# Performance work log

Measured on AMD Instinct MI355X. Metric: run time of the kernel, lower is better.

Reference implementation:

```python
import jax, jax.numpy as jnp
import numpy as np

IN_FEATURES = 4096
OUT_FEATURES = 16384
SCALE = 0.02


def setup_inputs() -> dict:
    key = jax.random.key(0)
    kx, kw, kb = jax.random.split(key, 3)
    x = jax.random.normal(kx, (4, 2048, IN_FEATURES), dtype=jnp.float32)
    # int8-valued quantized weight, stored as int32 (values in [-127, 127])
    q_weight = jax.random.randint(kw, (OUT_FEATURES, IN_FEATURES), -127, 128, dtype=jnp.int32)
    scale = jnp.float32(SCALE)
    bias = jax.random.normal(kb, (OUT_FEATURES,), dtype=jnp.float32)
    return {"x": x, "q_weight": q_weight, "scale": scale, "bias": bias}


def reference(x, q_weight, scale, bias):
    # weight = q_weight.float() * scale  (dequantize)
    weight = q_weight.astype(jnp.float32) * scale  # [out, in]
    # F.linear(x, weight, bias) = x @ weight.T + bias
    out = jnp.einsum('bsi,oi->bso', x, weight) + bias
    return out
```

## Files before the change

kernel.cpp:

```cpp
#include <hip/hip_runtime.h>
#include <stdint.h>

#define K_DIM 4096
#define N_DIM 16384
#define M_DIM 8192

typedef _Float16 half8 __attribute__((ext_vector_type(8)));
typedef float floatx4 __attribute__((ext_vector_type(4)));

__device__ inline void gld_lds16(const void* g, void* l) {
  __builtin_amdgcn_global_load_lds(
      (const __attribute__((address_space(1))) void*)g,
      (__attribute__((address_space(3))) void*)l, 16, 0, 0);
}

__global__ __launch_bounds__(256) void cvt_f32_f16_k(const float* __restrict__ in,
                                                     _Float16* __restrict__ out) {
  size_t idx = (size_t)blockIdx.x * 256 + threadIdx.x;
  const float4* p = (const float4*)in + idx * 2;
  float4 v0 = p[0], v1 = p[1];
  half8 h;
  h[0] = (_Float16)v0.x; h[1] = (_Float16)v0.y; h[2] = (_Float16)v0.z; h[3] = (_Float16)v0.w;
  h[4] = (_Float16)v1.x; h[5] = (_Float16)v1.y; h[6] = (_Float16)v1.z; h[7] = (_Float16)v1.w;
  *((half8*)out + idx) = h;
}

__global__ __launch_bounds__(256) void cvt_i32_f16_k(const int* __restrict__ in,
                                                     _Float16* __restrict__ out) {
  size_t idx = (size_t)blockIdx.x * 256 + threadIdx.x;
  const int4* p = (const int4*)in + idx * 2;
  int4 v0 = p[0], v1 = p[1];
  half8 h;
  h[0] = (_Float16)v0.x; h[1] = (_Float16)v0.y; h[2] = (_Float16)v0.z; h[3] = (_Float16)v0.w;
  h[4] = (_Float16)v1.x; h[5] = (_Float16)v1.y; h[6] = (_Float16)v1.z; h[7] = (_Float16)v1.w;
  *((half8*)out + idx) = h;
}

template <bool FROM_WS>
__global__ __launch_bounds__(256) void qgemm_k(const void* __restrict__ Av,
                                               const void* __restrict__ Bv,
                                               const float* __restrict__ scale_p,
                                               const float* __restrict__ bias,
                                               float* __restrict__ out) {
  constexpr int BK = 64;
  __shared__ __align__(16) _Float16 sA[128 * BK];
  __shared__ __align__(16) _Float16 sB[128 * BK];

  const int tid  = threadIdx.x;
  const int lane = tid & 63;
  const int wid  = tid >> 6;
  const int wm   = wid >> 1, wn = wid & 1;
  const int q    = lane >> 4;
  const int l15  = lane & 15;
  const int bn   = blockIdx.x, bm = blockIdx.y;

  int gI[4], rI[4], cI[4];
#pragma unroll
  for (int p = 0; p < 4; ++p) {
    int g = p * 256 + tid;
    gI[p] = g;
    rI[p] = g >> 3;
    cI[p] = (g & 7) ^ (rI[p] & 7);
  }

  floatx4 acc[4][4] = {};

  const int arow = wm * 64 + l15;
  const int brow = wn * 64 + l15;

  const _Float16* Ah = nullptr; const _Float16* Bh = nullptr;
  const float* Af = nullptr;    const int* Bq = nullptr;
  if constexpr (FROM_WS) { Ah = (const _Float16*)Av; Bh = (const _Float16*)Bv; }
  else                   { Af = (const float*)Av;    Bq = (const int*)Bv; }

#pragma unroll 1
  for (int k0 = 0; k0 < K_DIM; k0 += BK) {
    if constexpr (FROM_WS) {
#pragma unroll
      for (int p = 0; p < 4; ++p)
        gld_lds16(Ah + (size_t)(bm * 128 + rI[p]) * K_DIM + k0 + cI[p] * 8,
                  &sA[gI[p] * 8]);
#pragma unroll
      for (int p = 0; p < 4; ++p)
        gld_lds16(Bh + (size_t)(bn * 128 + rI[p]) * K_DIM + k0 + cI[p] * 8,
                  &sB[gI[p] * 8]);
    } else {
#pragma unroll
      for (int p = 0; p < 4; ++p) {
        const float4* pa =
            (const float4*)(Af + (size_t)(bm * 128 + rI[p]) * K_DIM + k0 + cI[p] * 8);
        float4 v0 = pa[0], v1 = pa[1];
        half8 h;
        h[0] = (_Float16)v0.x; h[1] = (_Float16)v0.y; h[2] = (_Float16)v0.z; h[3] = (_Float16)v0.w;
        h[4] = (_Float16)v1.x; h[5] = (_Float16)v1.y; h[6] = (_Float16)v1.z; h[7] = (_Float16)v1.w;
        *(half8*)&sA[gI[p] * 8] = h;
      }
#pragma unroll
      for (int p = 0; p < 4; ++p) {
        const int4* pb =
            (const int4*)(Bq + (size_t)(bn * 128 + rI[p]) * K_DIM + k0 + cI[p] * 8);
        int4 v0 = pb[0], v1 = pb[1];
        half8 h;
        h[0] = (_Float16)v0.x; h[1] = (_Float16)v0.y; h[2] = (_Float16)v0.z; h[3] = (_Float16)v0.w;
        h[4] = (_Float16)v1.x; h[5] = (_Float16)v1.y; h[6] = (_Float16)v1.z; h[7] = (_Float16)v1.w;
        *(half8*)&sB[gI[p] * 8] = h;
      }
    }
    __syncthreads();

#pragma unroll
    for (int kk = 0; kk < BK; kk += 32) {
      const int xt = ((((kk >> 3) + q) ^ (lane & 7)) * 8);
      half8 af[4], bf[4];
#pragma unroll
      for (int i = 0; i < 4; ++i) af[i] = *(const half8*)&sA[(arow + i * 16) * BK + xt];
#pragma unroll
      for (int j = 0; j < 4; ++j) bf[j] = *(const half8*)&sB[(brow + j * 16) * BK + xt];
#pragma unroll
      for (int i = 0; i < 4; ++i)
#pragma unroll
        for (int j = 0; j < 4; ++j)
          acc[i][j] = __builtin_amdgcn_mfma_f32_16x16x32_f16(af[i], bf[j], acc[i][j], 0, 0, 0);
    }
    __syncthreads();
  }

  const float s = *scale_p;
  float bv[4];
#pragma unroll
  for (int j = 0; j < 4; ++j) bv[j] = bias[bn * 128 + wn * 64 + j * 16 + l15];
  const int mb = bm * 128 + wm * 64 + q * 4;
  const size_t nb = (size_t)bn * 128 + wn * 64 + l15;
#pragma unroll
  for (int i = 0; i < 4; ++i) {
#pragma unroll
    for (int j = 0; j < 4; ++j) {
      size_t off = (size_t)(mb + i * 16) * N_DIM + nb + j * 16;
      floatx4 c = acc[i][j];
      out[off]             = c[0] * s + bv[j];
      out[off + N_DIM]     = c[1] * s + bv[j];
      out[off + 2 * N_DIM] = c[2] * s + bv[j];
      out[off + 3 * N_DIM] = c[3] * s + bv[j];
    }
  }
}

extern "C" void kernel_launch(void* const* d_in, const int* in_sizes, int n_in,
                              void* d_out, int out_size, void* d_ws, size_t ws_size,
                              hipStream_t stream) {
  const float* x     = (const float*)d_in[0];
  const int*   qw    = (const int*)d_in[1];
  const float* scale = (const float*)d_in[2];
  const float* bias  = (const float*)d_in[3];
  float* out = (float*)d_out;

  const size_t xs  = (size_t)M_DIM * K_DIM;
  const size_t wsz = (size_t)N_DIM * K_DIM;
  const size_t need = (xs + wsz) * sizeof(_Float16);

  dim3 grid(N_DIM / 128, M_DIM / 128);
  if (ws_size >= need) {
    _Float16* xh = (_Float16*)d_ws;
    _Float16* wh = xh + xs;
    cvt_f32_f16_k<<<(int)(xs / 8 / 256), 256, 0, stream>>>(x, xh);
    cvt_i32_f16_k<<<(int)(wsz / 8 / 256), 256, 0, stream>>>(qw, wh);
    qgemm_k<true><<<grid, 256, 0, stream>>>(xh, wh, scale, bias, out);
  } else {
    qgemm_k<false><<<grid, 256, 0, stream>>>(x, qw, scale, bias, out);
  }
}
```

Measured before the change: 2.129 ms.

## Add 256x256 double-buffered GEMM kernel with interleaved async LDS staging

Adds a new fp16 MFMA GEMM kernel for the workspace path. It uses 256x256 tiles with 512 threads and double-buffered LDS. Global-to-LDS loads for the next tiles are interleaved between MFMA phases, with explicit waitcnt, barriers and setprio. It also remaps block indices to improve L2 reuse. The aim is to raise arithmetic intensity and hide memory latency behind compute, at the cost of 128KB of LDS, heavy register use, and many barriers per iteration.

```diff
diff --git a/kernel.cpp b/kernel.cpp
--- a/kernel.cpp
+++ b/kernel.cpp
@@ -36,6 +36,139 @@
   *((half8*)out + idx) = h;
 }
 
+__global__ __launch_bounds__(512, 2) void qgemm256_k(
+    const _Float16* __restrict__ Ah, const _Float16* __restrict__ Bh,
+    const float* __restrict__ scale_p, const float* __restrict__ bias,
+    float* __restrict__ out) {
+  constexpr int BK = 64;
+  constexpr int NT = K_DIM / BK;
+  __shared__ __align__(16) _Float16 sA[2][256 * BK];
+  __shared__ __align__(16) _Float16 sB[2][256 * BK];
+
+  const int tid  = threadIdx.x;
+  const int lane = tid & 63;
+  const int wid  = tid >> 6;
+  const int wm   = wid >> 2;
+  const int wn   = wid & 3;
+  const int q    = lane >> 4;
+  const int l15  = lane & 15;
+
+  const int nbn = N_DIM / 256;
+  int lin = blockIdx.y * gridDim.x + blockIdx.x;
+  int swz = (lin & 7) * ((M_DIM / 256) * nbn / 8) + (lin >> 3);
+  const int bn = swz % nbn;
+  const int bm = swz / nbn;
+
+  const int s_slot = tid & 7;
+  const int r0     = tid >> 3;
+  const int cc     = s_slot ^ (r0 & 7);
+  const _Float16* Agp = Ah + (size_t)(bm * 256 + r0) * K_DIM + cc * 8;
+  const _Float16* Bgp = Bh + (size_t)(bn * 256 + r0) * K_DIM + cc * 8;
+
+#define STAGE_A(b, tt, h)                                                        \
+  { const _Float16* s_ = Agp + (size_t)(h) * 128 * K_DIM + (tt) * BK;            \
+    gld_lds16(s_, &sA[(b)][(h) * 8192 + tid * 8]);                               \
+    gld_lds16(s_ + (size_t)64 * K_DIM, &sA[(b)][(h) * 8192 + 4096 + tid * 8]); }
+#define STAGE_B(b, tt, h)                                                        \
+  { const _Float16* s_ = Bgp + (size_t)(h) * 128 * K_DIM + (tt) * BK;            \
+    gld_lds16(s_, &sB[(b)][(h) * 8192 + tid * 8]);                               \
+    gld_lds16(s_ + (size_t)64 * K_DIM, &sB[(b)][(h) * 8192 + 4096 + tid * 8]); }
+#define MFMA16(d, a_, b_) d = __builtin_amdgcn_mfma_f32_16x16x32_f16(a_, b_, d, 0, 0, 0)
+#define SBAR() __builtin_amdgcn_sched_barrier(0)
+#define BARRIER() { SBAR(); __builtin_amdgcn_s_barrier(); SBAR(); }
+
+  const int rbA = (wm * 128 + l15) * BK;
+  const int rbB = (wn * 64 + l15) * BK;
+  const int xt0 = (q ^ (l15 & 7)) * 8;
+  const int xt1 = ((q + 4) ^ (l15 & 7)) * 8;
+
+  floatx4 acc[8][4] = {};
+
+  STAGE_A(0, 0, 0); STAGE_A(0, 0, 1);
+  STAGE_B(0, 0, 0); STAGE_B(0, 0, 1);
+  STAGE_A(1, 1, 0); STAGE_A(1, 1, 1);
+  asm volatile("s_waitcnt vmcnt(4)" ::: "memory");
+  BARRIER();
+
+#pragma unroll 1
+  for (int t = 0; t < NT; ++t) {
+    const int buf = t & 1;
+    const _Float16* pa = sA[buf];
+    const _Float16* pb = sB[buf];
+    half8 a0[8], a1[8], b0[4], b1[4];
+
+    b0[0] = *(const half8*)&pb[rbB + xt0];
+    b0[1] = *(const half8*)&pb[rbB + 1024 + xt0];
+#pragma unroll
+    for (int i = 0; i < 8; ++i) a0[i] = *(const half8*)&pa[rbA + i * 1024 + xt0];
+    if (t < NT - 1) STAGE_B(buf ^ 1, t + 1, 0);
+    BARRIER();
+    __builtin_amdgcn_s_setprio(1);
+#pragma unroll
+    for (int i = 0; i < 8; ++i) { MFMA16(acc[i][0], a0[i], b0[0]); MFMA16(acc[i][1], a0[i], b0[1]); }
+    __builtin_amdgcn_s_setprio(0);
+    BARRIER();
+
+    b0[2] = *(const half8*)&pb[rbB + 2048 + xt0];
+    b0[3] = *(const half8*)&pb[rbB + 3072 + xt0];
+#pragma unroll
+    for (int i = 0; i < 8; ++i) a1[i] = *(const half8*)&pa[rbA + i * 1024 + xt1];
+    if (t < NT - 1) STAGE_B(buf ^ 1, t + 1, 1);
+    BARRIER();
+    __builtin_amdgcn_s_setprio(1);
+#pragma unroll
+    for (int i = 0; i < 8; ++i) { MFMA16(acc[i][2], a0[i], b0[2]); MFMA16(acc[i][3], a0[i], b0[3]); }
+    __builtin_amdgcn_s_setprio(0);
+    BARRIER();
+
+    b1[0] = *(const half8*)&pb[rbB + xt1];
+    b1[1] = *(const half8*)&pb[rbB + 1024 + xt1];
+    if (t < NT - 2) STAGE_A(buf, t + 2, 0);
+    BARRIER();
+    __builtin_amdgcn_s_setprio(1);
+#pragma unroll
+    for (int i = 0; i < 8; ++i) { MFMA16(acc[i][0], a1[i], b1[0]); MFMA16(acc[i][1], a1[i], b1[1]); }
+    __builtin_amdgcn_s_setprio(0);
+    BARRIER();
+
+    b1[2] = *(const half8*)&pb[rbB + 2048 + xt1];
+    b1[3] = *(const half8*)&pb[rbB + 3072 + xt1];
+    if (t < NT - 2) STAGE_A(buf, t + 2, 1);
+    BARRIER();
+    __builtin_amdgcn_s_setprio(1);
+#pragma unroll
+    for (int i = 0; i < 8; ++i) { MFMA16(acc[i][2], a1[i], b1[2]); MFMA16(acc[i][3], a1[i], b1[3]); }
+    __builtin_amdgcn_s_setprio(0);
+    if (t < NT - 2) { asm volatile("s_waitcnt vmcnt(4)" ::: "memory"); }
+    else            { asm volatile("s_waitcnt vmcnt(0)" ::: "memory"); }
+    BARRIER();
+  }
+
+  const float s = *scale_p;
+  float bv[4];
+#pragma unroll
+  for (int j = 0; j < 4; ++j) bv[j] = bias[bn * 256 + wn * 64 + j * 16 + l15];
+  const int mb = bm * 256 + wm * 128 + q * 4;
+  const size_t nb = (size_t)bn * 256 + wn * 64 + l15;
+#pragma unroll
+  for (int i = 0; i < 8; ++i) {
+#pragma unroll
+    for (int j = 0; j < 4; ++j) {
+      size_t off = (size_t)(mb + i * 16) * N_DIM + nb + j * 16;
+      floatx4 c = acc[i][j];
+      out[off]             = c[0] * s + bv[j];
+      out[off + N_DIM]     = c[1] * s + bv[j];
+      out[off + 2 * N_DIM] = c[2] * s + bv[j];
+      out[off + 3 * N_DIM] = c[3] * s + bv[j];
+    }
+  }
+#undef STAGE_A
+#undef STAGE_B
+#undef MFMA16
+#undef SBAR
+#undef BARRIER
+}
+
 template <bool FROM_WS>
 __global__ __launch_bounds__(256) void qgemm_k(const void* __restrict__ Av,
                                                const void* __restrict__ Bv,
@@ -68,22 +201,20 @@
   const int arow = wm * 64 + l15;
   const int brow = wn * 64 + l15;
 
-  const _Float16* Ah = nullptr; const _Float16* Bh = nullptr;
-  const float* Af = nullptr;    const int* Bq = nullptr;
-  if constexpr (FROM_WS) { Ah = (const _Float16*)Av; Bh = (const _Float16*)Bv; }
-  else                   { Af = (const float*)Av;    Bq = (const int*)Bv; }
+  const _Float16* Ahp = nullptr; const _Float16* Bhp = nullptr;
+  const float* Af = nullptr;     const int* Bq = nullptr;
+  if constexpr (FROM_WS) { Ahp = (const _Float16*)Av; Bhp = (const _Float16*)Bv; }
+  else                   { Af = (const float*)Av;     Bq = (const int*)Bv; }
 
 #pragma unroll 1
   for (int k0 = 0; k0 < K_DIM; k0 += BK) {
     if constexpr (FROM_WS) {
 #pragma unroll
       for (int p = 0; p < 4; ++p)
-        gld_lds16(Ah + (size_t)(bm * 128 + rI[p]) * K_DIM + k0 + cI[p] * 8,
-                  &sA[gI[p] * 8]);
+        gld_lds16(Ahp + (size_t)(bm * 128 + rI[p]) * K_DIM + k0 + cI[p] * 8, &sA[gI[p] * 8]);
 #pragma unroll
       for (int p = 0; p < 4; ++p)
-        gld_lds16(Bh + (size_t)(bn * 128 + rI[p]) * K_DIM + k0 + cI[p] * 8,
-                  &sB[gI[p] * 8]);
+        gld_lds16(Bhp + (size_t)(bn * 128 + rI[p]) * K_DIM + k0 + cI[p] * 8, &sB[gI[p] * 8]);
     } else {
 #pragma unroll
       for (int p = 0; p < 4; ++p) {
@@ -158,14 +289,15 @@
   const size_t wsz = (size_t)N_DIM * K_DIM;
   const size_t need = (xs + wsz) * sizeof(_Float16);
 
-  dim3 grid(N_DIM / 128, M_DIM / 128);
   if (ws_size >= need) {
     _Float16* xh = (_Float16*)d_ws;
     _Float16* wh = xh + xs;
     cvt_f32_f16_k<<<(int)(xs / 8 / 256), 256, 0, stream>>>(x, xh);
     cvt_i32_f16_k<<<(int)(wsz / 8 / 256), 256, 0, stream>>>(qw, wh);
-    qgemm_k<true><<<grid, 256, 0, stream>>>(xh, wh, scale, bias, out);
+    dim3 grid(N_DIM / 256, M_DIM / 256);
+    qgemm256_k<<<grid, 512, 0, stream>>>(xh, wh, scale, bias, out);
   } else {
+    dim3 grid(N_DIM / 128, M_DIM / 128);
     qgemm_k<false><<<grid, 256, 0, stream>>>(x, qw, scale, bias, out);
   }
 }
```

After: 1.827 ms. -14.2%, faster.
